# Optimization experiments

Measured on AMD Instinct MI355X. Metric: run time of the kernel, lower is better.

The kernel has to match this reference:

```python
import jax, jax.numpy as jnp
import numpy as np

EMBED_DIM = 384
NUM_HEADS = 6
HEAD_DIM = EMBED_DIM // NUM_HEADS
SCALE = HEAD_DIM ** (-0.5)


def setup_inputs() -> dict:
    key = jax.random.key(0)
    ks = jax.random.split(key, 5)
    B, N, D = 8, 2048, EMBED_DIM
    x = jax.random.normal(ks[0], (B, N, D), dtype=jnp.float32)
    # Linear params, torch convention: weight [out, in], bias [out]
    w_qkv = jax.random.normal(ks[1], (3 * D, D), dtype=jnp.float32) * (D ** -0.5)
    b_qkv = jax.random.normal(ks[2], (3 * D,), dtype=jnp.float32) * 0.01
    w_out = jax.random.normal(ks[3], (D, D), dtype=jnp.float32) * (D ** -0.5)
    b_out = jax.random.normal(ks[4], (D,), dtype=jnp.float32) * 0.01
    return {"x": x, "w_qkv": w_qkv, "b_qkv": b_qkv, "w_out": w_out, "b_out": b_out}


def reference(x, w_qkv, b_qkv, w_out, b_out):
    B, N, D = x.shape
    H, Dh = NUM_HEADS, HEAD_DIM
    # qkv projection: [B,N,3D]
    qkv = jnp.einsum('bnd,ed->bne', x, w_qkv) + b_qkv
    qkv = qkv.reshape(B, N, 3, H, Dh).transpose(2, 0, 3, 1, 4)  # [3,B,H,N,Dh]
    q, k, v = qkv[0], qkv[1], qkv[2]
    # full NxN attention scores (faithful to original eager math)
    scores = jnp.einsum('bhnd,bhmd->bhnm', q, k) * SCALE  # [B,H,N,N]
    attn = jax.nn.softmax(scores, axis=-1)
    out = jnp.einsum('bhnm,bhmd->bhnd', attn, v)  # [B,H,N,Dh]
    out = out.transpose(0, 2, 1, 3).reshape(B, N, D)
    out = jnp.einsum('bnd,ed->bne', out, w_out) + b_out
    return out
```

## Files before the change

### kernel.cpp

```cpp
#include <hip/hip_runtime.h>

typedef unsigned short u16;
typedef float f32x4 __attribute__((ext_vector_type(4)));
typedef __bf16 bf16x8 __attribute__((ext_vector_type(8)));
typedef unsigned short u16x8 __attribute__((ext_vector_type(8)));
typedef unsigned short u16x4 __attribute__((ext_vector_type(4)));

__device__ inline u16 f2bf(float f) {
    return __builtin_bit_cast(u16, (__bf16)f);
}

#define MFMA(a, b, c) __builtin_amdgcn_mfma_f32_16x16x32_bf16((a), (b), (c), 0, 0, 0)

#define C_SHIFT 17.3123405f
#define Q_SCALE 0.1803368801f

__global__ __launch_bounds__(256)
void cvt_kernel(const float* __restrict__ X, const float* __restrict__ Wq,
                const float* __restrict__ Wo, u16* __restrict__ Xb,
                u16* __restrict__ Wqb, u16* __restrict__ Wob)
{
    int i = blockIdx.x * 256 + threadIdx.x;
    const float* src; u16* dst; int off;
    if (i < 1572864)       { src = X;  dst = Xb;  off = i; }
    else if (i < 1683456)  { src = Wq; dst = Wqb; off = i - 1572864; }
    else                   { src = Wo; dst = Wob; off = i - 1683456; }
    f32x4 v = *(const f32x4*)&src[off * 4];
    u16x4 p;
    for (int k = 0; k < 4; ++k) p[k] = f2bf(v[k]);
    *(u16x4*)&dst[off * 4] = p;
}

__global__ __launch_bounds__(256)
void qkv_kernel(const u16* __restrict__ Xb, const u16* __restrict__ Wqb,
                const float* __restrict__ B, u16* __restrict__ Qo,
                u16* __restrict__ Ko, u16* __restrict__ VTo)
{
    __shared__ __align__(16) u16 As[64][72];
    __shared__ __align__(16) u16 Ws[64][72];
    const int tid = threadIdx.x;
    const int m0 = blockIdx.x * 64;
    const int n0 = blockIdx.y * 64;
    const int wv = tid >> 6, lane = tid & 63;
    const int l15 = lane & 15, quad = lane >> 4;

    f32x4 acc[4] = {};
    for (int kt = 0; kt < 384; kt += 64) {
        __syncthreads();
        for (int c = tid; c < 512; c += 256) {
            int row = c >> 3, cc = (c & 7) * 8;
            *(u16x8*)&As[row][cc] = *(const u16x8*)&Xb[(m0 + row) * 384 + kt + cc];
            *(u16x8*)&Ws[row][cc] = *(const u16x8*)&Wqb[(n0 + row) * 384 + kt + cc];
        }
        __syncthreads();
        for (int kc = 0; kc < 2; ++kc) {
            bf16x8 b = *(const bf16x8*)&Ws[wv * 16 + l15][kc * 32 + quad * 8];
            for (int mi = 0; mi < 4; ++mi) {
                bf16x8 a = *(const bf16x8*)&As[mi * 16 + l15][kc * 32 + quad * 8];
                acc[mi] = MFMA(a, b, acc[mi]);
            }
        }
    }
    const int col = n0 + wv * 16 + l15;
    const int t = col / 384;
    const int h = (col % 384) / 64;
    const int dh = col & 63;
    const float bias = B[col];
    for (int mi = 0; mi < 4; ++mi) {
        for (int r = 0; r < 4; ++r) {
            int gm = m0 + mi * 16 + quad * 4 + r;
            int bb = gm >> 11, n = gm & 2047;
            int bh = bb * 6 + h;
            float v = acc[mi][r] + bias;
            if (t == 0)      Qo[(bh * 2048 + n) * 64 + dh] = f2bf(v * Q_SCALE);
            else if (t == 1) Ko[(bh * 2048 + n) * 64 + dh] = f2bf(v);
            else             VTo[(bh * 64 + dh) * 2048 + n] = f2bf(v);
        }
    }
}

__global__ __launch_bounds__(512)
void attn_kernel(const u16* __restrict__ Q, const u16* __restrict__ K,
                 const u16* __restrict__ VT, u16* __restrict__ O)
{
    __shared__ __align__(16) u16 Ks[64][72];
    __shared__ __align__(16) u16 VTs[64][72];
    __shared__ __align__(16) u16 Pbuf[128][72];

    const int tid = threadIdx.x;
    const int bh = blockIdx.y;
    const int q0 = blockIdx.x * 128;
    const int wv = tid >> 6, lane = tid & 63;
    const int l15 = lane & 15, quad = lane >> 4;
    const int qrow = wv * 16 + l15;

    const u16* qptr = &Q[(bh * 2048 + q0 + qrow) * 64 + quad * 8];
    bf16x8 qf0 = *(const bf16x8*)qptr;
    bf16x8 qf1 = *(const bf16x8*)(qptr + 32);

    const int srow = tid >> 3, scc = (tid & 7) * 8;
    const u16* kbase = &K[(bh * 2048 + srow) * 64 + scc];
    const u16* vbase = &VT[(bh * 64 + srow) * 2048 + scc];

    const f32x4 cinit = {-C_SHIFT, -C_SHIFT, -C_SHIFT, -C_SHIFT};
    float l_part = 0.f;
    f32x4 acc[4] = {};

    u16x8 kreg = *(const u16x8*)kbase;
    u16x8 vreg = *(const u16x8*)vbase;

    for (int j = 0; j < 32; ++j) {
        __syncthreads();
        *(u16x8*)&Ks[srow][scc]  = kreg;
        *(u16x8*)&VTs[srow][scc] = vreg;
        __syncthreads();
        if (j < 31) {
            kreg = *(const u16x8*)(kbase + (j + 1) * 4096);
            vreg = *(const u16x8*)(vbase + (j + 1) * 64);
        }

        for (int ct = 0; ct < 4; ++ct) {
            bf16x8 a0 = *(const bf16x8*)&Ks[ct * 16 + l15][quad * 8];
            bf16x8 a1 = *(const bf16x8*)&Ks[ct * 16 + l15][32 + quad * 8];
            f32x4 s = MFMA(a0, qf0, cinit);
            s = MFMA(a1, qf1, s);
            u16x4 pk;
            for (int r = 0; r < 4; ++r) {
                float p = __builtin_amdgcn_exp2f(s[r]);
                l_part += p;
                pk[r] = f2bf(p);
            }
            *(u16x4*)&Pbuf[qrow][ct * 16 + quad * 4] = pk;
        }

        bf16x8 p0 = *(const bf16x8*)&Pbuf[qrow][quad * 8];
        bf16x8 p1 = *(const bf16x8*)&Pbuf[qrow][32 + quad * 8];
        for (int ct = 0; ct < 4; ++ct) {
            bf16x8 b0 = *(const bf16x8*)&VTs[ct * 16 + l15][quad * 8];
            bf16x8 b1 = *(const bf16x8*)&VTs[ct * 16 + l15][32 + quad * 8];
            acc[ct] = MFMA(p0, b0, acc[ct]);
            acc[ct] = MFMA(p1, b1, acc[ct]);
        }
    }

    float l_row = l_part;
    l_row += __shfl_xor(l_row, 16);
    l_row += __shfl_xor(l_row, 32);
    int b = bh / 6, h = bh % 6;
    float li[4];
    for (int r = 0; r < 4; ++r) li[r] = 1.0f / __shfl(l_row, quad * 4 + r);
    for (int ct = 0; ct < 4; ++ct)
        for (int r = 0; r < 4; ++r) {
            int row = q0 + wv * 16 + quad * 4 + r;
            int dh = ct * 16 + l15;
            O[(b * 2048 + row) * 384 + h * 64 + dh] = f2bf(acc[ct][r] * li[r]);
        }
}

__global__ __launch_bounds__(256)
void outproj_kernel(const u16* __restrict__ A, const u16* __restrict__ Wob,
                    const float* __restrict__ B, float* __restrict__ out)
{
    __shared__ __align__(16) u16 As[64][72];
    __shared__ __align__(16) u16 Ws[64][72];
    const int tid = threadIdx.x;
    const int m0 = blockIdx.x * 64;
    const int n0 = blockIdx.y * 64;
    const int wv = tid >> 6, lane = tid & 63;
    const int l15 = lane & 15, quad = lane >> 4;

    f32x4 acc[4] = {};
    for (int kt = 0; kt < 384; kt += 64) {
        __syncthreads();
        for (int c = tid; c < 512; c += 256) {
            int row = c >> 3, cc = (c & 7) * 8;
            *(u16x8*)&As[row][cc] = *(const u16x8*)&A[(m0 + row) * 384 + kt + cc];
            *(u16x8*)&Ws[row][cc] = *(const u16x8*)&Wob[(n0 + row) * 384 + kt + cc];
        }
        __syncthreads();
        for (int kc = 0; kc < 2; ++kc) {
            bf16x8 b = *(const bf16x8*)&Ws[wv * 16 + l15][kc * 32 + quad * 8];
            for (int mi = 0; mi < 4; ++mi) {
                bf16x8 a = *(const bf16x8*)&As[mi * 16 + l15][kc * 32 + quad * 8];
                acc[mi] = MFMA(a, b, acc[mi]);
            }
        }
    }
    const int col = n0 + wv * 16 + l15;
    const float bias = B[col];
    for (int mi = 0; mi < 4; ++mi)
        for (int r = 0; r < 4; ++r) {
            int gm = m0 + mi * 16 + quad * 4 + r;
            out[gm * 384 + col] = acc[mi][r] + bias;
        }
}

extern "C" void kernel_launch(void* const* d_in, const int* in_sizes, int n_in,
                              void* d_out, int out_size, void* d_ws, size_t ws_size,
                              hipStream_t stream) {
    const float* x     = (const float*)d_in[0];
    const float* w_qkv = (const float*)d_in[1];
    const float* b_qkv = (const float*)d_in[2];
    const float* w_out = (const float*)d_in[3];
    const float* b_out = (const float*)d_in[4];
    float* out = (float*)d_out;

    char* ws = (char*)d_ws;
    u16* Qw   = (u16*)(ws);
    u16* Kw   = (u16*)(ws + 12582912);
    u16* VTw  = (u16*)(ws + 25165824);
    u16* XbAw = (u16*)(ws + 37748736);
    u16* Wqb  = (u16*)(ws + 50331648);
    u16* Wob  = (u16*)(ws + 51216384);

    cvt_kernel<<<6720, 256, 0, stream>>>(x, w_qkv, w_out, XbAw, Wqb, Wob);
    qkv_kernel<<<dim3(256, 18), 256, 0, stream>>>(XbAw, Wqb, b_qkv, Qw, Kw, VTw);
    attn_kernel<<<dim3(16, 48), 512, 0, stream>>>(Qw, Kw, VTw, XbAw);
    outproj_kernel<<<dim3(256, 6), 256, 0, stream>>>(XbAw, Wob, b_out, out);
}
```

Baseline: 209.6 us.

## Enlarge per-wave register tiles in QKV GEMM and attention kernels

The QKV projection moves to 128x128 block tiles, with each wave computing a 64x64 sub-tile so that A and B fragments loaded from LDS are reused across a 4x4 grid of MFMAs. The attention kernel drops from 8 waves to 2 waves per block, and each wave now handles 64 query rows instead of 16. This reuses every K/V fragment read from LDS across four query blocks. The aim is to cut LDS traffic per MFMA, at the cost of higher register pressure, fewer waves per block and less latency hiding.

```diff
diff --git a/kernel.cpp b/kernel.cpp
--- a/kernel.cpp
+++ b/kernel.cpp
@@ -36,50 +36,56 @@
                 const float* __restrict__ B, u16* __restrict__ Qo,
                 u16* __restrict__ Ko, u16* __restrict__ VTo)
 {
-    __shared__ __align__(16) u16 As[64][72];
-    __shared__ __align__(16) u16 Ws[64][72];
+    __shared__ __align__(16) u16 As[128][72];
+    __shared__ __align__(16) u16 Ws[128][72];
     const int tid = threadIdx.x;
-    const int m0 = blockIdx.x * 64;
-    const int n0 = blockIdx.y * 64;
+    const int m0 = blockIdx.x * 128;
+    const int n0 = blockIdx.y * 128;
     const int wv = tid >> 6, lane = tid & 63;
     const int l15 = lane & 15, quad = lane >> 4;
-
-    f32x4 acc[4] = {};
+    const int mw = (wv & 1) * 64, nw = (wv >> 1) * 64;
+    const int srow = tid >> 3, scc = (tid & 7) * 8;
+
+    f32x4 acc[4][4] = {};
     for (int kt = 0; kt < 384; kt += 64) {
         __syncthreads();
-        for (int c = tid; c < 512; c += 256) {
-            int row = c >> 3, cc = (c & 7) * 8;
-            *(u16x8*)&As[row][cc] = *(const u16x8*)&Xb[(m0 + row) * 384 + kt + cc];
-            *(u16x8*)&Ws[row][cc] = *(const u16x8*)&Wqb[(n0 + row) * 384 + kt + cc];
+        for (int i = 0; i < 4; ++i) {
+            *(u16x8*)&As[srow + i * 32][scc] =
+                *(const u16x8*)&Xb[(m0 + srow + i * 32) * 384 + kt + scc];
+            *(u16x8*)&Ws[srow + i * 32][scc] =
+                *(const u16x8*)&Wqb[(n0 + srow + i * 32) * 384 + kt + scc];
         }
         __syncthreads();
         for (int kc = 0; kc < 2; ++kc) {
-            bf16x8 b = *(const bf16x8*)&Ws[wv * 16 + l15][kc * 32 + quad * 8];
-            for (int mi = 0; mi < 4; ++mi) {
-                bf16x8 a = *(const bf16x8*)&As[mi * 16 + l15][kc * 32 + quad * 8];
-                acc[mi] = MFMA(a, b, acc[mi]);
-            }
-        }
-    }
-    const int col = n0 + wv * 16 + l15;
-    const int t = col / 384;
-    const int h = (col % 384) / 64;
-    const int dh = col & 63;
-    const float bias = B[col];
-    for (int mi = 0; mi < 4; ++mi) {
-        for (int r = 0; r < 4; ++r) {
-            int gm = m0 + mi * 16 + quad * 4 + r;
-            int bb = gm >> 11, n = gm & 2047;
-            int bh = bb * 6 + h;
-            float v = acc[mi][r] + bias;
-            if (t == 0)      Qo[(bh * 2048 + n) * 64 + dh] = f2bf(v * Q_SCALE);
-            else if (t == 1) Ko[(bh * 2048 + n) * 64 + dh] = f2bf(v);
-            else             VTo[(bh * 64 + dh) * 2048 + n] = f2bf(v);
-        }
-    }
-}
-
-__global__ __launch_bounds__(512)
+            bf16x8 a[4], bf[4];
+            for (int mi = 0; mi < 4; ++mi)
+                a[mi] = *(const bf16x8*)&As[mw + mi * 16 + l15][kc * 32 + quad * 8];
+            for (int nj = 0; nj < 4; ++nj)
+                bf[nj] = *(const bf16x8*)&Ws[nw + nj * 16 + l15][kc * 32 + quad * 8];
+            for (int mi = 0; mi < 4; ++mi)
+                for (int nj = 0; nj < 4; ++nj)
+                    acc[mi][nj] = MFMA(a[mi], bf[nj], acc[mi][nj]);
+        }
+    }
+    for (int nj = 0; nj < 4; ++nj) {
+        int col = n0 + nw + nj * 16 + l15;
+        int t = col / 384;
+        int h = (col % 384) / 64, dh = col & 63;
+        float bias = B[col];
+        for (int mi = 0; mi < 4; ++mi)
+            for (int r = 0; r < 4; ++r) {
+                int gm = m0 + mw + mi * 16 + quad * 4 + r;
+                int bb = gm >> 11, n = gm & 2047;
+                int bh = bb * 6 + h;
+                float v = acc[mi][nj][r] + bias;
+                if (t == 0)      Qo[(bh * 2048 + n) * 64 + dh] = f2bf(v * Q_SCALE);
+                else if (t == 1) Ko[(bh * 2048 + n) * 64 + dh] = f2bf(v);
+                else             VTo[(bh * 64 + dh) * 2048 + n] = f2bf(v);
+            }
+    }
+}
+
+__global__ __launch_bounds__(128)
 void attn_kernel(const u16* __restrict__ Q, const u16* __restrict__ K,
                  const u16* __restrict__ VT, u16* __restrict__ O)
 {
@@ -92,69 +98,88 @@
     const int q0 = blockIdx.x * 128;
     const int wv = tid >> 6, lane = tid & 63;
     const int l15 = lane & 15, quad = lane >> 4;
-    const int qrow = wv * 16 + l15;
-
-    const u16* qptr = &Q[(bh * 2048 + q0 + qrow) * 64 + quad * 8];
-    bf16x8 qf0 = *(const bf16x8*)qptr;
-    bf16x8 qf1 = *(const bf16x8*)(qptr + 32);
+
+    bf16x8 qf[4][2];
+    for (int qb = 0; qb < 4; ++qb) {
+        const u16* qptr = &Q[(bh * 2048 + q0 + wv * 64 + qb * 16 + l15) * 64 + quad * 8];
+        qf[qb][0] = *(const bf16x8*)qptr;
+        qf[qb][1] = *(const bf16x8*)(qptr + 32);
+    }
 
     const int srow = tid >> 3, scc = (tid & 7) * 8;
     const u16* kbase = &K[(bh * 2048 + srow) * 64 + scc];
     const u16* vbase = &VT[(bh * 64 + srow) * 2048 + scc];
 
     const f32x4 cinit = {-C_SHIFT, -C_SHIFT, -C_SHIFT, -C_SHIFT};
-    float l_part = 0.f;
-    f32x4 acc[4] = {};
-
-    u16x8 kreg = *(const u16x8*)kbase;
-    u16x8 vreg = *(const u16x8*)vbase;
+    float l_part[4] = {};
+    f32x4 acc[4][4] = {};
+
+    u16x8 kreg[4], vreg[4];
+    for (int i = 0; i < 4; ++i) {
+        kreg[i] = *(const u16x8*)(kbase + i * 1024);
+        vreg[i] = *(const u16x8*)(vbase + i * 32768);
+    }
 
     for (int j = 0; j < 32; ++j) {
         __syncthreads();
-        *(u16x8*)&Ks[srow][scc]  = kreg;
-        *(u16x8*)&VTs[srow][scc] = vreg;
+        for (int i = 0; i < 4; ++i) {
+            *(u16x8*)&Ks[srow + i * 16][scc]  = kreg[i];
+            *(u16x8*)&VTs[srow + i * 16][scc] = vreg[i];
+        }
         __syncthreads();
         if (j < 31) {
-            kreg = *(const u16x8*)(kbase + (j + 1) * 4096);
-            vreg = *(const u16x8*)(vbase + (j + 1) * 64);
+            for (int i = 0; i < 4; ++i) {
+                kreg[i] = *(const u16x8*)(kbase + (j + 1) * 4096 + i * 1024);
+                vreg[i] = *(const u16x8*)(vbase + (j + 1) * 64 + i * 32768);
+            }
         }
 
         for (int ct = 0; ct < 4; ++ct) {
             bf16x8 a0 = *(const bf16x8*)&Ks[ct * 16 + l15][quad * 8];
             bf16x8 a1 = *(const bf16x8*)&Ks[ct * 16 + l15][32 + quad * 8];
-            f32x4 s = MFMA(a0, qf0, cinit);
-            s = MFMA(a1, qf1, s);
-            u16x4 pk;
-            for (int r = 0; r < 4; ++r) {
-                float p = __builtin_amdgcn_exp2f(s[r]);
-                l_part += p;
-                pk[r] = f2bf(p);
-            }
-            *(u16x4*)&Pbuf[qrow][ct * 16 + quad * 4] = pk;
-        }
-
-        bf16x8 p0 = *(const bf16x8*)&Pbuf[qrow][quad * 8];
-        bf16x8 p1 = *(const bf16x8*)&Pbuf[qrow][32 + quad * 8];
+            for (int qb = 0; qb < 4; ++qb) {
+                f32x4 s = MFMA(a0, qf[qb][0], cinit);
+                s = MFMA(a1, qf[qb][1], s);
+                u16x4 pk;
+                for (int r = 0; r < 4; ++r) {
+                    float p = __builtin_amdgcn_exp2f(s[r]);
+                    l_part[qb] += p;
+                    pk[r] = f2bf(p);
+                }
+                *(u16x4*)&Pbuf[wv * 64 + qb * 16 + l15][ct * 16 + quad * 4] = pk;
+            }
+        }
+
+        bf16x8 pf[4][2];
+        for (int qb = 0; qb < 4; ++qb) {
+            const u16* pp = &Pbuf[wv * 64 + qb * 16 + l15][quad * 8];
+            pf[qb][0] = *(const bf16x8*)pp;
+            pf[qb][1] = *(const bf16x8*)(pp + 32);
+        }
         for (int ct = 0; ct < 4; ++ct) {
             bf16x8 b0 = *(const bf16x8*)&VTs[ct * 16 + l15][quad * 8];
             bf16x8 b1 = *(const bf16x8*)&VTs[ct * 16 + l15][32 + quad * 8];
-            acc[ct] = MFMA(p0, b0, acc[ct]);
-            acc[ct] = MFMA(p1, b1, acc[ct]);
-        }
-    }
-
-    float l_row = l_part;
-    l_row += __shfl_xor(l_row, 16);
-    l_row += __shfl_xor(l_row, 32);
+            for (int qb = 0; qb < 4; ++qb) {
+                acc[qb][ct] = MFMA(pf[qb][0], b0, acc[qb][ct]);
+                acc[qb][ct] = MFMA(pf[qb][1], b1, acc[qb][ct]);
+            }
+        }
+    }
+
     int b = bh / 6, h = bh % 6;
-    float li[4];
-    for (int r = 0; r < 4; ++r) li[r] = 1.0f / __shfl(l_row, quad * 4 + r);
-    for (int ct = 0; ct < 4; ++ct)
-        for (int r = 0; r < 4; ++r) {
-            int row = q0 + wv * 16 + quad * 4 + r;
-            int dh = ct * 16 + l15;
-            O[(b * 2048 + row) * 384 + h * 64 + dh] = f2bf(acc[ct][r] * li[r]);
-        }
+    for (int qb = 0; qb < 4; ++qb) {
+        float lr = l_part[qb];
+        lr += __shfl_xor(lr, 16);
+        lr += __shfl_xor(lr, 32);
+        float li[4];
+        for (int r = 0; r < 4; ++r) li[r] = 1.0f / __shfl(lr, quad * 4 + r);
+        for (int ct = 0; ct < 4; ++ct)
+            for (int r = 0; r < 4; ++r) {
+                int row = q0 + wv * 64 + qb * 16 + quad * 4 + r;
+                int dh = ct * 16 + l15;
+                O[(b * 2048 + row) * 384 + h * 64 + dh] = f2bf(acc[qb][ct][r] * li[r]);
+            }
+    }
 }
 
 __global__ __launch_bounds__(256)
@@ -214,7 +239,7 @@
     u16* Wob  = (u16*)(ws + 51216384);
 
     cvt_kernel<<<6720, 256, 0, stream>>>(x, w_qkv, w_out, XbAw, Wqb, Wob);
-    qkv_kernel<<<dim3(256, 18), 256, 0, stream>>>(XbAw, Wqb, b_qkv, Qw, Kw, VTw);
-    attn_kernel<<<dim3(16, 48), 512, 0, stream>>>(Qw, Kw, VTw, XbAw);
+    qkv_kernel<<<dim3(128, 9), 256, 0, stream>>>(XbAw, Wqb, b_qkv, Qw, Kw, VTw);
+    attn_kernel<<<dim3(16, 48), 128, 0, stream>>>(Qw, Kw, VTw, XbAw);
     outproj_kernel<<<dim3(256, 6), 256, 0, stream>>>(XbAw, Wob, b_out, out);
 }
```

Measured after the change: 252.9 us. 20.7% more time.
